# Kernel tuning notes

Hardware: AMD Instinct MI355X
Metric: run time of the kernel (lower is better)

## Reference

```python
import jax, jax.numpy as jnp
import numpy as np

N_NODES = 20000
N_EDGES = 320000
IN_DIM = 128
HID = 64
HEADS = 4
NEG_SLOPE = 0.2  # PyG GATConv default


def _glorot(key, shape):
    fan_in, fan_out = shape[0], shape[-1]
    lim = jnp.sqrt(6.0 / (fan_in + fan_out))
    return jax.random.uniform(key, shape, jnp.float32, -lim, lim)


def setup_inputs() -> dict:
    key = jax.random.key(0)
    ks = jax.random.split(key, 16)
    x = jax.random.normal(ks[0], (N_NODES, IN_DIM), jnp.float32)
    edge_index = jax.random.randint(ks[1], (2, N_EDGES), 0, N_NODES, dtype=jnp.int64)
    # layer 1: in=128 -> heads=4, out=64, concat
    W1 = _glorot(ks[2], (IN_DIM, HEADS * HID))
    a_src1 = _glorot(ks[3], (HEADS, HID))
    a_dst1 = _glorot(ks[4], (HEADS, HID))
    b1 = jnp.zeros((HEADS * HID,), jnp.float32)
    # layer 2: in=256 -> heads=4, out=64, concat
    W2 = _glorot(ks[5], (HEADS * HID, HEADS * HID))
    a_src2 = _glorot(ks[6], (HEADS, HID))
    a_dst2 = _glorot(ks[7], (HEADS, HID))
    b2 = jnp.zeros((HEADS * HID,), jnp.float32)
    # layer 3: in=256 -> heads=1, out=1, mean (concat=False)
    W3 = _glorot(ks[8], (HEADS * HID, 1))
    a_src3 = _glorot(ks[9], (1, 1))
    a_dst3 = _glorot(ks[10], (1, 1))
    b3 = jnp.zeros((1,), jnp.float32)
    return {
        "x": x, "edge_index": edge_index,
        "W1": W1, "a_src1": a_src1, "a_dst1": a_dst1, "b1": b1,
        "W2": W2, "a_src2": a_src2, "a_dst2": a_dst2, "b2": b2,
        "W3": W3, "a_src3": a_src3, "a_dst3": a_dst3, "b3": b3,
    }


def gat_conv(x, src, dst, W, a_src, a_dst, b, heads, out_c, concat):
    """PyG GATConv (add_self_loops already applied to src/dst)."""
    n = x.shape[0]
    h = (x @ W).reshape(n, heads, out_c)            # [N,H,C]
    alpha_s = jnp.sum(h * a_src, axis=-1)           # [N,H]
    alpha_d = jnp.sum(h * a_dst, axis=-1)           # [N,H]
    e = jax.nn.leaky_relu(alpha_s[src] + alpha_d[dst], NEG_SLOPE)  # [E,H]
    # segment softmax over incoming edges of each destination node
    e_max = jax.ops.segment_max(e, dst, num_segments=n)            # [N,H]
    ex = jnp.exp(e - e_max[dst])                                   # [E,H]
    denom = jax.ops.segment_sum(ex, dst, num_segments=n)           # [N,H]
    alpha = ex / denom[dst]                                        # [E,H]
    msg = h[src] * alpha[:, :, None]                               # [E,H,C]
    out = jax.ops.segment_sum(msg, dst, num_segments=n)            # [N,H,C]
    if concat:
        out = out.reshape(n, heads * out_c)
    else:
        out = out.mean(axis=1)
    return out + b


def reference(x, edge_index, W1, a_src1, a_dst1, b1, W2, a_src2, a_dst2, b2,
              W3, a_src3, a_dst3, b3):
    n = x.shape[0]
    loops = jnp.arange(n, dtype=edge_index.dtype)
    src = jnp.concatenate([edge_index[0], loops])
    dst = jnp.concatenate([edge_index[1], loops])
    h = jax.nn.elu(gat_conv(x, src, dst, W1, a_src1, a_dst1, b1, HEADS, HID, True))
    # dropout is identity in eval mode
    h = jax.nn.elu(gat_conv(h, src, dst, W2, a_src2, a_dst2, b2, HEADS, HID, True))
    h = gat_conv(h, src, dst, W3, a_src3, a_dst3, b3, 1, 1, False)
    return h.reshape(-1)
```

## Files before the change

kernel.cpp:

```cpp
#include <hip/hip_runtime.h>
#include <hip/hip_bf16.h>
#include <cmath>

#define N_NODESC 20000
#define E_RAW    320000
#define E_TOTC   340000
#define HEADSC   4
#define FC       256
#define NEG_SLOPE 0.2f

typedef __attribute__((ext_vector_type(8))) short short8v;
typedef __attribute__((ext_vector_type(4))) float f32x4;

__device__ __forceinline__ int dstOf(const int* ei, int e) {
  return (e < E_RAW) ? ei[E_RAW + e] : (e - E_RAW);
}
__device__ __forceinline__ int srcOf(const int* ei, int e) {
  return (e < E_RAW) ? ei[e] : (e - E_RAW);
}
__device__ __forceinline__ float lrelu(float v) { return v > 0.f ? v : NEG_SLOPE * v; }

__device__ __forceinline__ unsigned short f2bf(float f) {
  __hip_bfloat16 h = __float2bfloat16(f);
  return reinterpret_cast<unsigned short&>(h);
}
__device__ __forceinline__ float bf2f(unsigned short u) {
  return __uint_as_float(((unsigned int)u) << 16);
}

__global__ void prep_split(const float* __restrict__ in, unsigned short* __restrict__ hi,
                           unsigned short* __restrict__ lo, int n) {
  int i = blockIdx.x * 256 + threadIdx.x;
  if (i >= n) return;
  float v = in[i];
  unsigned short h = f2bf(v);
  hi[i] = h;
  lo[i] = f2bf(v - bf2f(h));
}

template<int K>
__global__ void prep_wt(const float* __restrict__ W, unsigned short* __restrict__ hiT,
                        unsigned short* __restrict__ loT) {
  int idx = blockIdx.x * 256 + threadIdx.x;
  if (idx >= 256 * K) return;
  int c = idx / K, k = idx - c * K;
  float v = W[(long)k * FC + c];
  unsigned short h = f2bf(v);
  hiT[(long)c * K + k] = h;
  loT[(long)c * K + k] = f2bf(v - bf2f(h));
}

template<int K>
__global__ void __launch_bounds__(256) mfma_gemm(
    const unsigned short* __restrict__ Ahi, const unsigned short* __restrict__ Alo,
    const unsigned short* __restrict__ WhiT, const unsigned short* __restrict__ WloT,
    const float* __restrict__ a_src, const float* __restrict__ a_dst,
    unsigned short* __restrict__ hb, float* __restrict__ as, float* __restrict__ ad) {
  __shared__ float asred[64][4];
  __shared__ float adred[64][4];
  const int t = threadIdx.x;
  const int w = t >> 6, l = t & 63;
  const int n0 = blockIdx.x * 64;
  const int r16 = l & 15;
  const int kq = l >> 4;
  const int col0 = w * 64;

  f32x4 acc[4][4];
#pragma unroll
  for (int rt = 0; rt < 4; ++rt)
#pragma unroll
    for (int ct = 0; ct < 4; ++ct) acc[rt][ct] = f32x4{0.f, 0.f, 0.f, 0.f};

  long arow[4];
#pragma unroll
  for (int rt = 0; rt < 4; ++rt) {
    int r = n0 + rt * 16 + r16;
    if (r >= N_NODESC) r = N_NODESC - 1;
    arow[rt] = (long)r * K;
  }

  for (int ks = 0; ks < K; ks += 32) {
    const int kb = ks + kq * 8;
    short8v aHi[4], aLo[4];
#pragma unroll
    for (int rt = 0; rt < 4; ++rt) {
      aHi[rt] = *(const short8v*)(Ahi + arow[rt] + kb);
      aLo[rt] = *(const short8v*)(Alo + arow[rt] + kb);
    }
#pragma unroll
    for (int ct = 0; ct < 4; ++ct) {
      const long wrow = (long)(col0 + ct * 16 + r16) * K + kb;
      short8v wHi = *(const short8v*)(WhiT + wrow);
      short8v wLo = *(const short8v*)(WloT + wrow);
#pragma unroll
      for (int rt = 0; rt < 4; ++rt) {
        acc[rt][ct] = __builtin_amdgcn_mfma_f32_16x16x32_bf16(aHi[rt], wHi, acc[rt][ct], 0, 0, 0);
        acc[rt][ct] = __builtin_amdgcn_mfma_f32_16x16x32_bf16(aHi[rt], wLo, acc[rt][ct], 0, 0, 0);
        acc[rt][ct] = __builtin_amdgcn_mfma_f32_16x16x32_bf16(aLo[rt], wHi, acc[rt][ct], 0, 0, 0);
      }
    }
  }

  float asv[4], adv[4];
#pragma unroll
  for (int ct = 0; ct < 4; ++ct) {
    int c = col0 + ct * 16 + r16;
    asv[ct] = a_src[c];
    adv[ct] = a_dst[c];
  }
#pragma unroll
  for (int rt = 0; rt < 4; ++rt) {
#pragma unroll
    for (int j = 0; j < 4; ++j) {
      const int r = rt * 16 + kq * 4 + j;
      const int g = n0 + r;
      if (g < N_NODESC) {
#pragma unroll
        for (int ct = 0; ct < 4; ++ct)
          hb[(long)g * FC + col0 + ct * 16 + r16] = f2bf(acc[rt][ct][j]);
      }
      float ps = acc[rt][0][j] * asv[0] + acc[rt][1][j] * asv[1]
               + acc[rt][2][j] * asv[2] + acc[rt][3][j] * asv[3];
      float pd = acc[rt][0][j] * adv[0] + acc[rt][1][j] * adv[1]
               + acc[rt][2][j] * adv[2] + acc[rt][3][j] * adv[3];
      for (int off = 8; off; off >>= 1) {
        ps += __shfl_down(ps, off, 16);
        pd += __shfl_down(pd, off, 16);
      }
      if (r16 == 0) {
        asred[r][w] = ps;
        adred[r][w] = pd;
      }
    }
  }
  __syncthreads();
  {
    const int rr = t >> 2, hh = t & 3;
    const int g = n0 + rr;
    if (g < N_NODESC) {
      as[(long)g * HEADSC + hh] = asred[rr][hh];
      ad[(long)g * HEADSC + hh] = adred[rr][hh];
    }
  }
}

__global__ void gemm3_kernel(const unsigned short* __restrict__ act_hi,
                             const unsigned short* __restrict__ act_lo,
                             const float* __restrict__ W3,
                             const float* __restrict__ asc, const float* __restrict__ adc,
                             float* __restrict__ h3, float* __restrict__ as,
                             float* __restrict__ ad) {
  const int n = blockIdx.x;
  const int t = threadIdx.x;
  float a = bf2f(act_hi[(long)n * FC + t]) + bf2f(act_lo[(long)n * FC + t]);
  float v = a * W3[t];
  for (int off = 32; off; off >>= 1) v += __shfl_down(v, off, 64);
  __shared__ float red[4];
  if ((t & 63) == 0) red[t >> 6] = v;
  __syncthreads();
  if (t == 0) {
    float s = red[0] + red[1] + red[2] + red[3];
    h3[n] = s;
    as[n] = s * asc[0];
    ad[n] = s * adc[0];
  }
}

__global__ void zero_deg(int* __restrict__ deg) {
  int i = blockIdx.x * 256 + threadIdx.x;
  if (i < N_NODESC) deg[i] = 0;
}

__global__ void deg_count(const int* __restrict__ ei, int* __restrict__ deg) {
  int e = blockIdx.x * 256 + threadIdx.x;
  if (e >= E_TOTC) return;
  atomicAdd(&deg[dstOf(ei, e)], 1);
}

__global__ void scan_kernel(const int* __restrict__ deg, int* __restrict__ row_ptr,
                            int* __restrict__ cursor) {
  __shared__ int partial[1024];
  const int t = threadIdx.x;
  const int PER = (N_NODESC + 1023) / 1024;
  const int base = t * PER;
  int s = 0;
  for (int i = 0; i < PER; ++i) {
    int idx = base + i;
    if (idx < N_NODESC) s += deg[idx];
  }
  partial[t] = s;
  __syncthreads();
  for (int off = 1; off < 1024; off <<= 1) {
    int v = (t >= off) ? partial[t - off] : 0;
    __syncthreads();
    partial[t] += v;
    __syncthreads();
  }
  int run = (t == 0) ? 0 : partial[t - 1];
  for (int i = 0; i < PER; ++i) {
    int idx = base + i;
    if (idx < N_NODESC) {
      row_ptr[idx] = run;
      cursor[idx]  = run;
      run += deg[idx];
    }
  }
  if (t == 1023) row_ptr[N_NODESC] = run;
}

__global__ void fill_kernel(const int* __restrict__ ei, int* __restrict__ cursor,
                            int* __restrict__ col_src) {
  int e = blockIdx.x * 256 + threadIdx.x;
  if (e >= E_TOTC) return;
  int d = dstOf(ei, e);
  int pos = atomicAdd(&cursor[d], 1);
  col_src[pos] = srcOf(ei, e);
}

__global__ void softmax4_kernel(const int* __restrict__ row_ptr, const int* __restrict__ col_src,
                                const float4* __restrict__ as4, const float4* __restrict__ ad4,
                                float4* __restrict__ ebuf4, float4* __restrict__ denom4) {
  const int w = threadIdx.x >> 6, l = threadIdx.x & 63;
  const int n = blockIdx.x * 4 + w;
  if (n >= N_NODESC) return;
  const int j0 = row_ptr[n], j1 = row_ptr[n + 1];
  const float4 adv = ad4[n];
  float4 mx = float4{-INFINITY, -INFINITY, -INFINITY, -INFINITY};
  for (int j = j0 + l; j < j1; j += 64) {
    float4 a = as4[col_src[j]];
    float4 v;
    v.x = lrelu(a.x + adv.x); v.y = lrelu(a.y + adv.y);
    v.z = lrelu(a.z + adv.z); v.w = lrelu(a.w + adv.w);
    ebuf4[j] = v;
    mx.x = fmaxf(mx.x, v.x); mx.y = fmaxf(mx.y, v.y);
    mx.z = fmaxf(mx.z, v.z); mx.w = fmaxf(mx.w, v.w);
  }
  for (int off = 32; off; off >>= 1) {
    mx.x = fmaxf(mx.x, __shfl_xor(mx.x, off, 64));
    mx.y = fmaxf(mx.y, __shfl_xor(mx.y, off, 64));
    mx.z = fmaxf(mx.z, __shfl_xor(mx.z, off, 64));
    mx.w = fmaxf(mx.w, __shfl_xor(mx.w, off, 64));
  }
  float4 sm = float4{0.f, 0.f, 0.f, 0.f};
  for (int j = j0 + l; j < j1; j += 64) {
    float4 v = ebuf4[j];
    float4 e;
    e.x = expf(v.x - mx.x); e.y = expf(v.y - mx.y);
    e.z = expf(v.z - mx.z); e.w = expf(v.w - mx.w);
    ebuf4[j] = e;
    sm.x += e.x; sm.y += e.y; sm.z += e.z; sm.w += e.w;
  }
  for (int off = 32; off; off >>= 1) {
    sm.x += __shfl_xor(sm.x, off, 64);
    sm.y += __shfl_xor(sm.y, off, 64);
    sm.z += __shfl_xor(sm.z, off, 64);
    sm.w += __shfl_xor(sm.w, off, 64);
  }
  if (l == 0)
    denom4[n] = float4{1.f / sm.x, 1.f / sm.y, 1.f / sm.z, 1.f / sm.w};
}

__global__ void softmax1_kernel(const int* __restrict__ row_ptr, const int* __restrict__ col_src,
                                const float* __restrict__ as, const float* __restrict__ ad,
                                float* __restrict__ ebuf, float* __restrict__ denom) {
  const int w = threadIdx.x >> 6, l = threadIdx.x & 63;
  const int n = blockIdx.x * 4 + w;
  if (n >= N_NODESC) return;
  const int j0 = row_ptr[n], j1 = row_ptr[n + 1];
  const float adv = ad[n];
  float mx = -INFINITY;
  for (int j = j0 + l; j < j1; j += 64) {
    float v = lrelu(as[col_src[j]] + adv);
    ebuf[j] = v;
    mx = fmaxf(mx, v);
  }
  for (int off = 32; off; off >>= 1) mx = fmaxf(mx, __shfl_xor(mx, off, 64));
  float sm = 0.f;
  for (int j = j0 + l; j < j1; j += 64) {
    float e = expf(ebuf[j] - mx);
    ebuf[j] = e;
    sm += e;
  }
  for (int off = 32; off; off >>= 1) sm += __shfl_xor(sm, off, 64);
  if (l == 0) denom[n] = 1.f / sm;
}

template<bool ELU>
__global__ void agg_kernel(const int* __restrict__ row_ptr, const int* __restrict__ col_src,
                           const float* __restrict__ ebuf, const float* __restrict__ denom,
                           const unsigned short* __restrict__ hb, const float* __restrict__ b,
                           unsigned short* __restrict__ out_hi, unsigned short* __restrict__ out_lo) {
  const int d = blockIdx.x;
  const int t = threadIdx.x;
  const int h = t >> 5;
  const int j0 = row_ptr[d], j1 = row_ptr[d + 1];
  const ushort2* hb2 = (const ushort2*)hb;
  float a0 = 0.f, a1 = 0.f;
  int j = j0;
  for (; j + 8 <= j1; j += 8) {
    int     s[8];
    ushort2 v[8];
    float   w[8];
#pragma unroll
    for (int u = 0; u < 8; ++u) s[u] = col_src[j + u];
#pragma unroll
    for (int u = 0; u < 8; ++u) v[u] = hb2[(long)s[u] * 128 + t];
#pragma unroll
    for (int u = 0; u < 8; ++u) w[u] = ebuf[(j + u) * HEADSC + h];
#pragma unroll
    for (int u = 0; u < 8; ++u) {
      a0 = fmaf(w[u], bf2f(v[u].x), a0);
      a1 = fmaf(w[u], bf2f(v[u].y), a1);
    }
  }
  for (; j < j1; ++j) {
    ushort2 v = hb2[(long)col_src[j] * 128 + t];
    float w = ebuf[j * HEADSC + h];
    a0 = fmaf(w, bf2f(v.x), a0);
    a1 = fmaf(w, bf2f(v.y), a1);
  }
  float dn = denom[d * HEADSC + h];
  float o0 = a0 * dn + b[2 * t];
  float o1 = a1 * dn + b[2 * t + 1];
  if (ELU) {
    o0 = o0 > 0.f ? o0 : expm1f(o0);
    o1 = o1 > 0.f ? o1 : expm1f(o1);
  }
  ushort2 hi, lo;
  hi.x = f2bf(o0); lo.x = f2bf(o0 - bf2f(hi.x));
  hi.y = f2bf(o1); lo.y = f2bf(o1 - bf2f(hi.y));
  ((ushort2*)out_hi)[(long)d * 128 + t] = hi;
  ((ushort2*)out_lo)[(long)d * 128 + t] = lo;
}

__global__ void agg3_kernel(const int* __restrict__ row_ptr, const int* __restrict__ col_src,
                            const float* __restrict__ ebuf, const float* __restrict__ denom,
                            const float* __restrict__ h3, const float* __restrict__ b3,
                            float* __restrict__ out) {
  const int wv = threadIdx.x >> 6;
  const int l  = threadIdx.x & 63;
  const int d  = blockIdx.x * 4 + wv;
  if (d >= N_NODESC) return;
  const int j0 = row_ptr[d], j1 = row_ptr[d + 1];
  float acc = 0.f;
  for (int j = j0 + l; j < j1; j += 64)
    acc = fmaf(ebuf[j], h3[col_src[j]], acc);
  for (int off = 32; off; off >>= 1) acc += __shfl_down(acc, off, 64);
  if (l == 0) out[d] = acc * denom[d] + b3[0];
}

extern "C" void kernel_launch(void* const* d_in, const int* in_sizes, int n_in,
                              void* d_out, int out_size, void* d_ws, size_t ws_size,
                              hipStream_t stream) {
  const float* x    = (const float*)d_in[0];
  const int*   ei   = (const int*)d_in[1];
  const float* W1   = (const float*)d_in[2];
  const float* as1  = (const float*)d_in[3];
  const float* ad1  = (const float*)d_in[4];
  const float* b1   = (const float*)d_in[5];
  const float* W2   = (const float*)d_in[6];
  const float* as2  = (const float*)d_in[7];
  const float* ad2  = (const float*)d_in[8];
  const float* b2   = (const float*)d_in[9];
  const float* W3   = (const float*)d_in[10];
  const float* as3  = (const float*)d_in[11];
  const float* ad3  = (const float*)d_in[12];
  const float* b3   = (const float*)d_in[13];
  float* out = (float*)d_out;

  float* ws = (float*)d_ws;
  size_t off = 0;
  float* wAs   = ws + off; off += (size_t)N_NODESC * HEADSC;
  float* wAd   = ws + off; off += (size_t)N_NODESC * HEADSC;
  float* denom = ws + off; off += (size_t)N_NODESC * HEADSC;
  float* ebuf  = ws + off; off += (size_t)E_TOTC * HEADSC;
  float* h3    = ws + off; off += N_NODESC;
  int* deg     = (int*)(ws + off); off += N_NODESC;
  int* row_ptr = (int*)(ws + off); off += N_NODESC + 1;
  int* cursor  = (int*)(ws + off); off += N_NODESC;
  int* col_src = (int*)(ws + off); off += E_TOTC;
  off = (off + 3) & ~(size_t)3;
  unsigned short* hb     = (unsigned short*)(ws + off); off += (size_t)N_NODESC * 128;
  unsigned short* act_hi = (unsigned short*)(ws + off); off += (size_t)N_NODESC * 128;
  unsigned short* act_lo = (unsigned short*)(ws + off); off += (size_t)N_NODESC * 128;
  unsigned short* xhi    = (unsigned short*)(ws + off); off += (size_t)N_NODESC * 64;
  unsigned short* xlo    = (unsigned short*)(ws + off); off += (size_t)N_NODESC * 64;
  unsigned short* WhiT   = (unsigned short*)(ws + off); off += 32768;
  unsigned short* WloT   = (unsigned short*)(ws + off); off += 32768;

  const int gridE  = (E_TOTC + 255) / 256;
  const int gridN  = (N_NODESC + 255) / 256;
  const int gridN4 = (N_NODESC + 3) / 4;
  const int gemmG  = (N_NODESC + 63) / 64;

  zero_deg<<<gridN, 256, 0, stream>>>(deg);
  deg_count<<<gridE, 256, 0, stream>>>(ei, deg);
  scan_kernel<<<1, 1024, 0, stream>>>(deg, row_ptr, cursor);
  fill_kernel<<<gridE, 256, 0, stream>>>(ei, cursor, col_src);
  prep_split<<<(N_NODESC * 128 + 255) / 256, 256, 0, stream>>>(x, xhi, xlo, N_NODESC * 128);

  prep_wt<128><<<(256 * 128 + 255) / 256, 256, 0, stream>>>(W1, WhiT, WloT);
  mfma_gemm<128><<<gemmG, 256, 0, stream>>>(xhi, xlo, WhiT, WloT, as1, ad1, hb, wAs, wAd);
  softmax4_kernel<<<gridN4, 256, 0, stream>>>(row_ptr, col_src, (const float4*)wAs,
                                              (const float4*)wAd, (float4*)ebuf, (float4*)denom);
  agg_kernel<true><<<N_NODESC, 128, 0, stream>>>(row_ptr, col_src, ebuf, denom, hb, b1,
                                                 act_hi, act_lo);

  prep_wt<256><<<(256 * 256 + 255) / 256, 256, 0, stream>>>(W2, WhiT, WloT);
  mfma_gemm<256><<<gemmG, 256, 0, stream>>>(act_hi, act_lo, WhiT, WloT, as2, ad2, hb, wAs, wAd);
  softmax4_kernel<<<gridN4, 256, 0, stream>>>(row_ptr, col_src, (const float4*)wAs,
                                              (const float4*)wAd, (float4*)ebuf, (float4*)denom);
  agg_kernel<true><<<N_NODESC, 128, 0, stream>>>(row_ptr, col_src, ebuf, denom, hb, b2,
                                                 act_hi, act_lo);

  gemm3_kernel<<<N_NODESC, 256, 0, stream>>>(act_hi, act_lo, W3, as3, ad3, h3, wAs, wAd);
  softmax1_kernel<<<gridN4, 256, 0, stream>>>(row_ptr, col_src, wAs, wAd, ebuf, denom);
  agg3_kernel<<<gridN4, 256, 0, stream>>>(row_ptr, col_src, ebuf, denom, h3, b3, out);
}
```

Measured before the change: 260.3 us.

## Fuse segment softmax into aggregation kernels and merge prep launches

Merges the per-layer segment-softmax and aggregation kernels into one kernel per destination node. Edge attention weights now live in shared memory (up to 512 edges), with a recompute path for larger degrees, so the global ebuf/denom buffers and their round trips go away. The x/W split, the weight transposes and the degree zeroing are combined into a single prep launch, and layer 3 softmax and aggregation are fused too. The cost is extra syncthreads, shared-memory use that may lower occupancy, and recomputed exps for high-degree nodes.

Result: faster. 234.2 us (-10.1%).

```diff
diff --git a/kernel.cpp b/kernel.cpp
--- a/kernel.cpp
+++ b/kernel.cpp
@@ -8,6 +8,7 @@
 #define HEADSC   4
 #define FC       256
 #define NEG_SLOPE 0.2f
+#define MAXD     512
 
 typedef __attribute__((ext_vector_type(8))) short short8v;
 typedef __attribute__((ext_vector_type(4))) float f32x4;
@@ -28,26 +29,35 @@
   return __uint_as_float(((unsigned int)u) << 16);
 }
 
-__global__ void prep_split(const float* __restrict__ in, unsigned short* __restrict__ hi,
-                           unsigned short* __restrict__ lo, int n) {
-  int i = blockIdx.x * 256 + threadIdx.x;
-  if (i >= n) return;
-  float v = in[i];
-  unsigned short h = f2bf(v);
-  hi[i] = h;
-  lo[i] = f2bf(v - bf2f(h));
-}
-
-template<int K>
-__global__ void prep_wt(const float* __restrict__ W, unsigned short* __restrict__ hiT,
-                        unsigned short* __restrict__ loT) {
-  int idx = blockIdx.x * 256 + threadIdx.x;
-  if (idx >= 256 * K) return;
-  int c = idx / K, k = idx - c * K;
-  float v = W[(long)k * FC + c];
-  unsigned short h = f2bf(v);
-  hiT[(long)c * K + k] = h;
-  loT[(long)c * K + k] = f2bf(v - bf2f(h));
+__global__ void mega_prep(const float* __restrict__ x,
+                          unsigned short* __restrict__ xhi, unsigned short* __restrict__ xlo,
+                          const float* __restrict__ W1,
+                          unsigned short* __restrict__ w1hi, unsigned short* __restrict__ w1lo,
+                          const float* __restrict__ W2,
+                          unsigned short* __restrict__ w2hi, unsigned short* __restrict__ w2lo,
+                          int* __restrict__ deg) {
+  const int bid = blockIdx.x, t = threadIdx.x;
+  if (bid < 10000) {
+    int i = bid * 256 + t;
+    float v = x[i];
+    unsigned short hh = f2bf(v);
+    xhi[i] = hh; xlo[i] = f2bf(v - bf2f(hh));
+  } else if (bid < 10128) {
+    int idx = (bid - 10000) * 256 + t;
+    int c = idx >> 7, k = idx & 127;
+    float v = W1[k * FC + c];
+    unsigned short hh = f2bf(v);
+    w1hi[c * 128 + k] = hh; w1lo[c * 128 + k] = f2bf(v - bf2f(hh));
+  } else if (bid < 10384) {
+    int idx = (bid - 10128) * 256 + t;
+    int c = idx >> 8, k = idx & 255;
+    float v = W2[k * FC + c];
+    unsigned short hh = f2bf(v);
+    w2hi[c * 256 + k] = hh; w2lo[c * 256 + k] = f2bf(v - bf2f(hh));
+  } else {
+    int i = (bid - 10384) * 256 + t;
+    if (i < N_NODESC) deg[i] = 0;
+  }
 }
 
 template<int K>
@@ -166,11 +176,6 @@
   }
 }
 
-__global__ void zero_deg(int* __restrict__ deg) {
-  int i = blockIdx.x * 256 + threadIdx.x;
-  if (i < N_NODESC) deg[i] = 0;
-}
-
 __global__ void deg_count(const int* __restrict__ ei, int* __restrict__ deg) {
   int e = blockIdx.x * 256 + threadIdx.x;
   if (e >= E_TOTC) return;
@@ -217,21 +222,29 @@
   col_src[pos] = srcOf(ei, e);
 }
 
-__global__ void softmax4_kernel(const int* __restrict__ row_ptr, const int* __restrict__ col_src,
-                                const float4* __restrict__ as4, const float4* __restrict__ ad4,
-                                float4* __restrict__ ebuf4, float4* __restrict__ denom4) {
-  const int w = threadIdx.x >> 6, l = threadIdx.x & 63;
-  const int n = blockIdx.x * 4 + w;
-  if (n >= N_NODESC) return;
-  const int j0 = row_ptr[n], j1 = row_ptr[n + 1];
-  const float4 adv = ad4[n];
+template<bool ELU>
+__global__ void __launch_bounds__(128) fused_sa(
+    const int* __restrict__ row_ptr, const int* __restrict__ col_src,
+    const float4* __restrict__ as4, const float4* __restrict__ ad4,
+    const unsigned short* __restrict__ hb, const float* __restrict__ b,
+    unsigned short* __restrict__ out_hi, unsigned short* __restrict__ out_lo) {
+  const int d = blockIdx.x;
+  const int t = threadIdx.x;
+  const int l = t & 63, wv = t >> 6;
+  const int j0 = row_ptr[d], j1 = row_ptr[d + 1];
+  const int deg = j1 - j0;
+  __shared__ float4 wbuf[MAXD];
+  __shared__ float4 xred[2];
+  const float4 adv = ad4[d];
+
   float4 mx = float4{-INFINITY, -INFINITY, -INFINITY, -INFINITY};
-  for (int j = j0 + l; j < j1; j += 64) {
+  for (int j = j0 + t; j < j1; j += 128) {
     float4 a = as4[col_src[j]];
     float4 v;
     v.x = lrelu(a.x + adv.x); v.y = lrelu(a.y + adv.y);
     v.z = lrelu(a.z + adv.z); v.w = lrelu(a.w + adv.w);
-    ebuf4[j] = v;
+    int jj = j - j0;
+    if (jj < MAXD) wbuf[jj] = v;
     mx.x = fmaxf(mx.x, v.x); mx.y = fmaxf(mx.y, v.y);
     mx.z = fmaxf(mx.z, v.z); mx.w = fmaxf(mx.w, v.w);
   }
@@ -241,13 +254,29 @@
     mx.z = fmaxf(mx.z, __shfl_xor(mx.z, off, 64));
     mx.w = fmaxf(mx.w, __shfl_xor(mx.w, off, 64));
   }
+  if (l == 0) xred[wv] = mx;
+  __syncthreads();
+  {
+    float4 m0 = xred[0], m1 = xred[1];
+    mx.x = fmaxf(m0.x, m1.x); mx.y = fmaxf(m0.y, m1.y);
+    mx.z = fmaxf(m0.z, m1.z); mx.w = fmaxf(m0.w, m1.w);
+  }
+  __syncthreads();
+
   float4 sm = float4{0.f, 0.f, 0.f, 0.f};
-  for (int j = j0 + l; j < j1; j += 64) {
-    float4 v = ebuf4[j];
+  for (int j = j0 + t; j < j1; j += 128) {
+    int jj = j - j0;
+    float4 v;
+    if (jj < MAXD) v = wbuf[jj];
+    else {
+      float4 a = as4[col_src[j]];
+      v.x = lrelu(a.x + adv.x); v.y = lrelu(a.y + adv.y);
+      v.z = lrelu(a.z + adv.z); v.w = lrelu(a.w + adv.w);
+    }
     float4 e;
     e.x = expf(v.x - mx.x); e.y = expf(v.y - mx.y);
     e.z = expf(v.z - mx.z); e.w = expf(v.w - mx.w);
-    ebuf4[j] = e;
+    if (jj < MAXD) wbuf[jj] = e;
     sm.x += e.x; sm.y += e.y; sm.z += e.z; sm.w += e.w;
   }
   for (int off = 32; off; off >>= 1) {
@@ -256,72 +285,59 @@
     sm.z += __shfl_xor(sm.z, off, 64);
     sm.w += __shfl_xor(sm.w, off, 64);
   }
-  if (l == 0)
-    denom4[n] = float4{1.f / sm.x, 1.f / sm.y, 1.f / sm.z, 1.f / sm.w};
-}
-
-__global__ void softmax1_kernel(const int* __restrict__ row_ptr, const int* __restrict__ col_src,
-                                const float* __restrict__ as, const float* __restrict__ ad,
-                                float* __restrict__ ebuf, float* __restrict__ denom) {
-  const int w = threadIdx.x >> 6, l = threadIdx.x & 63;
-  const int n = blockIdx.x * 4 + w;
-  if (n >= N_NODESC) return;
-  const int j0 = row_ptr[n], j1 = row_ptr[n + 1];
-  const float adv = ad[n];
-  float mx = -INFINITY;
-  for (int j = j0 + l; j < j1; j += 64) {
-    float v = lrelu(as[col_src[j]] + adv);
-    ebuf[j] = v;
-    mx = fmaxf(mx, v);
-  }
-  for (int off = 32; off; off >>= 1) mx = fmaxf(mx, __shfl_xor(mx, off, 64));
-  float sm = 0.f;
-  for (int j = j0 + l; j < j1; j += 64) {
-    float e = expf(ebuf[j] - mx);
-    ebuf[j] = e;
-    sm += e;
-  }
-  for (int off = 32; off; off >>= 1) sm += __shfl_xor(sm, off, 64);
-  if (l == 0) denom[n] = 1.f / sm;
-}
-
-template<bool ELU>
-__global__ void agg_kernel(const int* __restrict__ row_ptr, const int* __restrict__ col_src,
-                           const float* __restrict__ ebuf, const float* __restrict__ denom,
-                           const unsigned short* __restrict__ hb, const float* __restrict__ b,
-                           unsigned short* __restrict__ out_hi, unsigned short* __restrict__ out_lo) {
-  const int d = blockIdx.x;
-  const int t = threadIdx.x;
+  if (l == 0) xred[wv] = sm;
+  __syncthreads();
+
   const int h = t >> 5;
-  const int j0 = row_ptr[d], j1 = row_ptr[d + 1];
+  float st0, mxh, advh;
+  {
+    float4 s0 = xred[0], s1 = xred[1];
+    float sx = s0.x + s1.x, sy = s0.y + s1.y, sz = s0.z + s1.z, sw = s0.w + s1.w;
+    st0  = (h == 0) ? sx : (h == 1) ? sy : (h == 2) ? sz : sw;
+    mxh  = (h == 0) ? mx.x : (h == 1) ? mx.y : (h == 2) ? mx.z : mx.w;
+    advh = (h == 0) ? adv.x : (h == 1) ? adv.y : (h == 2) ? adv.z : adv.w;
+  }
+  const float dnh = 1.f / st0;
+
+  const float* wlds = (const float*)wbuf;
   const ushort2* hb2 = (const ushort2*)hb;
   float a0 = 0.f, a1 = 0.f;
-  int j = j0;
-  for (; j + 8 <= j1; j += 8) {
-    int     s[8];
-    ushort2 v[8];
-    float   w[8];
-#pragma unroll
-    for (int u = 0; u < 8; ++u) s[u] = col_src[j + u];
-#pragma unroll
-    for (int u = 0; u < 8; ++u) v[u] = hb2[(long)s[u] * 128 + t];
-#pragma unroll
-    for (int u = 0; u < 8; ++u) w[u] = ebuf[(j + u) * HEADSC + h];
-#pragma unroll
-    for (int u = 0; u < 8; ++u) {
-      a0 = fmaf(w[u], bf2f(v[u].x), a0);
-      a1 = fmaf(w[u], bf2f(v[u].y), a1);
-    }
-  }
-  for (; j < j1; ++j) {
-    ushort2 v = hb2[(long)col_src[j] * 128 + t];
-    float w = ebuf[j * HEADSC + h];
-    a0 = fmaf(w, bf2f(v.x), a0);
-    a1 = fmaf(w, bf2f(v.y), a1);
-  }
-  float dn = denom[d * HEADSC + h];
-  float o0 = a0 * dn + b[2 * t];
-  float o1 = a1 * dn + b[2 * t + 1];
+  if (deg <= MAXD) {
+    int j = j0;
+    for (; j + 8 <= j1; j += 8) {
+      int     s[8];
+      ushort2 v[8];
+      float   w[8];
+#pragma unroll
+      for (int u = 0; u < 8; ++u) s[u] = col_src[j + u];
+#pragma unroll
+      for (int u = 0; u < 8; ++u) v[u] = hb2[(long)s[u] * 128 + t];
+#pragma unroll
+      for (int u = 0; u < 8; ++u) w[u] = wlds[(j + u - j0) * 4 + h];
+#pragma unroll
+      for (int u = 0; u < 8; ++u) {
+        a0 = fmaf(w[u], bf2f(v[u].x), a0);
+        a1 = fmaf(w[u], bf2f(v[u].y), a1);
+      }
+    }
+    for (; j < j1; ++j) {
+      ushort2 v = hb2[(long)col_src[j] * 128 + t];
+      float w = wlds[(j - j0) * 4 + h];
+      a0 = fmaf(w, bf2f(v.x), a0);
+      a1 = fmaf(w, bf2f(v.y), a1);
+    }
+  } else {
+    const float* asf = (const float*)as4;
+    for (int j = j0; j < j1; ++j) {
+      int s = col_src[j];
+      float e = expf(lrelu(asf[s * 4 + h] + advh) - mxh);
+      ushort2 v = hb2[(long)s * 128 + t];
+      a0 = fmaf(e, bf2f(v.x), a0);
+      a1 = fmaf(e, bf2f(v.y), a1);
+    }
+  }
+  float o0 = a0 * dnh + b[2 * t];
+  float o1 = a1 * dnh + b[2 * t + 1];
   if (ELU) {
     o0 = o0 > 0.f ? o0 : expm1f(o0);
     o1 = o1 > 0.f ? o1 : expm1f(o1);
@@ -333,20 +349,32 @@
   ((ushort2*)out_lo)[(long)d * 128 + t] = lo;
 }
 
-__global__ void agg3_kernel(const int* __restrict__ row_ptr, const int* __restrict__ col_src,
-                            const float* __restrict__ ebuf, const float* __restrict__ denom,
-                            const float* __restrict__ h3, const float* __restrict__ b3,
-                            float* __restrict__ out) {
-  const int wv = threadIdx.x >> 6;
-  const int l  = threadIdx.x & 63;
-  const int d  = blockIdx.x * 4 + wv;
+__global__ void __launch_bounds__(256) fused_sa3(
+    const int* __restrict__ row_ptr, const int* __restrict__ col_src,
+    const float* __restrict__ as, const float* __restrict__ ad,
+    const float* __restrict__ h3, const float* __restrict__ b3,
+    float* __restrict__ out) {
+  const int wv = threadIdx.x >> 6, l = threadIdx.x & 63;
+  const int d = blockIdx.x * 4 + wv;
   if (d >= N_NODESC) return;
   const int j0 = row_ptr[d], j1 = row_ptr[d + 1];
-  float acc = 0.f;
+  const float adv = ad[d];
+  float mx = -INFINITY;
   for (int j = j0 + l; j < j1; j += 64)
-    acc = fmaf(ebuf[j], h3[col_src[j]], acc);
-  for (int off = 32; off; off >>= 1) acc += __shfl_down(acc, off, 64);
-  if (l == 0) out[d] = acc * denom[d] + b3[0];
+    mx = fmaxf(mx, lrelu(as[col_src[j]] + adv));
+  for (int off = 32; off; off >>= 1) mx = fmaxf(mx, __shfl_xor(mx, off, 64));
+  float sm = 0.f, acc = 0.f;
+  for (int j = j0 + l; j < j1; j += 64) {
+    int s = col_src[j];
+    float e = expf(lrelu(as[s] + adv) - mx);
+    sm += e;
+    acc = fmaf(e, h3[s], acc);
+  }
+  for (int off = 32; off; off >>= 1) {
+    sm  += __shfl_xor(sm, off, 64);
+    acc += __shfl_xor(acc, off, 64);
+  }
+  if (l == 0) out[d] = acc / sm + b3[0];
 }
 
 extern "C" void kernel_launch(void* const* d_in, const int* in_sizes, int n_in,
@@ -372,8 +400,6 @@
   size_t off = 0;
   float* wAs   = ws + off; off += (size_t)N_NODESC * HEADSC;
   float* wAd   = ws + off; off += (size_t)N_NODESC * HEADSC;
-  float* denom = ws + off; off += (size_t)N_NODESC * HEADSC;
-  float* ebuf  = ws + off; off += (size_t)E_TOTC * HEADSC;
   float* h3    = ws + off; off += N_NODESC;
   int* deg     = (int*)(ws + off); off += N_NODESC;
   int* row_ptr = (int*)(ws + off); off += N_NODESC + 1;
@@ -385,35 +411,29 @@
   unsigned short* act_lo = (unsigned short*)(ws + off); off += (size_t)N_NODESC * 128;
   unsigned short* xhi    = (unsigned short*)(ws + off); off += (size_t)N_NODESC * 64;
   unsigned short* xlo    = (unsigned short*)(ws + off); off += (size_t)N_NODESC * 64;
-  unsigned short* WhiT   = (unsigned short*)(ws + off); off += 32768;
-  unsigned short* WloT   = (unsigned short*)(ws + off); off += 32768;
+  unsigned short* W1hiT  = (unsigned short*)(ws + off); off += 16384;
+  unsigned short* W1loT  = (unsigned short*)(ws + off); off += 16384;
+  unsigned short* W2hiT  = (unsigned short*)(ws + off); off += 32768;
+  unsigned short* W2loT  = (unsigned short*)(ws + off); off += 32768;
 
   const int gridE  = (E_TOTC + 255) / 256;
-  const int gridN  = (N_NODESC + 255) / 256;
   const int gridN4 = (N_NODESC + 3) / 4;
   const int gemmG  = (N_NODESC + 63) / 64;
 
-  zero_deg<<<gridN, 256, 0, stream>>>(deg);
+  mega_prep<<<10463, 256, 0, stream>>>(x, xhi, xlo, W1, W1hiT, W1loT,
+                                       W2, W2hiT, W2loT, deg);
   deg_count<<<gridE, 256, 0, stream>>>(ei, deg);
   scan_kernel<<<1, 1024, 0, stream>>>(deg, row_ptr, cursor);
   fill_kernel<<<gridE, 256, 0, stream>>>(ei, cursor, col_src);
-  prep_split<<<(N_NODESC * 128 + 255) / 256, 256, 0, stream>>>(x, xhi, xlo, N_NODESC * 128);
-
-  prep_wt<128><<<(256 * 128 + 255) / 256, 256, 0, stream>>>(W1, WhiT, WloT);
-  mfma_gemm<128><<<gemmG, 256, 0, stream>>>(xhi, xlo, WhiT, WloT, as1, ad1, hb, wAs, wAd);
-  softmax4_kernel<<<gridN4, 256, 0, stream>>>(row_ptr, col_src, (const float4*)wAs,
-                                              (const float4*)wAd, (float4*)ebuf, (float4*)denom);
-  agg_kernel<true><<<N_NODESC, 128, 0, stream>>>(row_ptr, col_src, ebuf, denom, hb, b1,
-                                                 act_hi, act_lo);
-
-  prep_wt<256><<<(256 * 256 + 255) / 256, 256, 0, stream>>>(W2, WhiT, WloT);
-  mfma_gemm<256><<<gemmG, 256, 0, stream>>>(act_hi, act_lo, WhiT, WloT, as2, ad2, hb, wAs, wAd);
-  softmax4_kernel<<<gridN4, 256, 0, stream>>>(row_ptr, col_src, (const float4*)wAs,
-                                              (const float4*)wAd, (float4*)ebuf, (float4*)denom);
-  agg_kernel<true><<<N_NODESC, 128, 0, stream>>>(row_ptr, col_src, ebuf, denom, hb, b2,
-                                                 act_hi, act_lo);
+
+  mfma_gemm<128><<<gemmG, 256, 0, stream>>>(xhi, xlo, W1hiT, W1loT, as1, ad1, hb, wAs, wAd);
+  fused_sa<true><<<N_NODESC, 128, 0, stream>>>(row_ptr, col_src, (const float4*)wAs,
+                                               (const float4*)wAd, hb, b1, act_hi, act_lo);
+
+  mfma_gemm<256><<<gemmG, 256, 0, stream>>>(act_hi, act_lo, W2hiT, W2loT, as2, ad2, hb, wAs, wAd);
+  fused_sa<true><<<N_NODESC, 128, 0, stream>>>(row_ptr, col_src, (const float4*)wAs,
+                                               (const float4*)wAd, hb, b2, act_hi, act_lo);
 
   gemm3_kernel<<<N_NODESC, 256, 0, stream>>>(act_hi, act_lo, W3, as3, ad3, h3, wAs, wAd);
-  softmax1_kernel<<<gridN4, 256, 0, stream>>>(row_ptr, col_src, wAs, wAd, ebuf, denom);
-  agg3_kernel<<<gridN4, 256, 0, stream>>>(row_ptr, col_src, ebuf, denom, h3, b3, out);
-}
+  fused_sa3<<<gridN4, 256, 0, stream>>>(row_ptr, col_src, wAs, wAd, h3, b3, out);
+}
```
